# Kernel tuning notes

Measured on AMD Instinct MI355X. Metric: run time of the kernel, lower is better.

The kernel has to match this reference:

```python
import jax, jax.numpy as jnp
import numpy as np

D_MODEL = 1024
N_HEADS = 16
D_K = D_MODEL // N_HEADS
NEG_INF = -1e30


def setup_inputs() -> dict:
    key = jax.random.key(0)
    ks = jax.random.split(key, 12)
    B, S = 4, 2048
    scale = 1.0 / np.sqrt(D_MODEL)
    inp = {
        "query": jax.random.normal(ks[0], (B, S, D_MODEL), jnp.float32),
        "key": jax.random.normal(ks[1], (B, S, D_MODEL), jnp.float32),
        "value": jax.random.normal(ks[2], (B, S, D_MODEL), jnp.float32),
        "mask": jax.random.randint(ks[3], (B, S, S), 0, 2, jnp.int32),
        "w_q": jax.random.normal(ks[4], (D_MODEL, D_MODEL), jnp.float32) * scale,
        "b_q": jnp.zeros((D_MODEL,), jnp.float32),
        "w_k": jax.random.normal(ks[5], (D_MODEL, D_MODEL), jnp.float32) * scale,
        "b_k": jnp.zeros((D_MODEL,), jnp.float32),
        "w_v": jax.random.normal(ks[6], (D_MODEL, D_MODEL), jnp.float32) * scale,
        "b_v": jnp.zeros((D_MODEL,), jnp.float32),
        "w_o": jax.random.normal(ks[7], (D_MODEL, D_MODEL), jnp.float32) * scale,
        "b_o": jnp.zeros((D_MODEL,), jnp.float32),
    }
    return inp


def reference(query, key, value, mask, w_q, b_q, w_k, b_k, w_v, b_v, w_o, b_o):
    B, Sq, _ = query.shape
    Sk = key.shape[1]
    # Linear projections (torch nn.Linear: x @ W.T + b), split into heads
    Q = (query @ w_q.T + b_q).reshape(B, Sq, N_HEADS, D_K).transpose(0, 2, 1, 3)
    K = (key @ w_k.T + b_k).reshape(B, Sk, N_HEADS, D_K).transpose(0, 2, 1, 3)
    V = (value @ w_v.T + b_v).reshape(B, Sk, N_HEADS, D_K).transpose(0, 2, 1, 3)
    # scores: (B, H, Sq, Sk)
    scores = jnp.einsum('bhqd,bhkd->bhqk', Q, K) / jnp.sqrt(jnp.float32(D_K))
    scores = jnp.where(mask[:, None, :, :] == 0, NEG_INF, scores)
    attn = jax.nn.softmax(scores, axis=-1)  # dropout p=0 -> identity (eval)
    context = jnp.einsum('bhqk,bhkd->bhqd', attn, V)
    context = context.transpose(0, 2, 1, 3).reshape(B, Sq, D_MODEL)
    return context @ w_o.T + b_o
```

## Files before the change

### kernel.cpp

```cpp
#include <hip/hip_runtime.h>
#include <hip/hip_bf16.h>
#include <stdint.h>

#define DM 1024
#define NHEADS 16
#define DK 64
#define BB 4
#define SS 2048

typedef unsigned short u16;
typedef __bf16 bf16x8 __attribute__((ext_vector_type(8)));
typedef __bf16 bf16x4 __attribute__((ext_vector_type(4)));
typedef float f32x4 __attribute__((ext_vector_type(4)));

#if __has_builtin(__builtin_amdgcn_exp2f)
#define EXP2(x) __builtin_amdgcn_exp2f(x)
#else
#define EXP2(x) exp2f(x)
#endif

static __device__ __forceinline__ u16 f2bf(float f) {
    union { float f; uint32_t u; } v; v.f = f;
    uint32_t r = v.u + 0x7fffu + ((v.u >> 16) & 1u);
    return (u16)(r >> 16);
}

static __device__ __forceinline__ f32x4 mfma16(bf16x8 a, bf16x8 b, f32x4 c) {
    return __builtin_amdgcn_mfma_f32_16x16x32_bf16(a, b, c, 0, 0, 0);
}

static __device__ __forceinline__ void gload16(const u16* g, u16* l) {
    __builtin_amdgcn_global_load_lds((const __attribute__((address_space(1))) void*)g,
                                     (__attribute__((address_space(3))) void*)l, 16, 0, 0);
}

#define PREP_W 4096
#define PREP_X 12288
#define PREP_M 2048
__global__ __launch_bounds__(256) void k_prep(const float* __restrict__ wq, const float* __restrict__ wk,
                                              const float* __restrict__ wv, const float* __restrict__ wo,
                                              u16* __restrict__ wout,
                                              const float* __restrict__ xq, const float* __restrict__ xk,
                                              const float* __restrict__ xv, u16* __restrict__ xout,
                                              const int* __restrict__ mask, uint32_t* __restrict__ bits) {
    const int bid = blockIdx.x, tid = threadIdx.x;
    if (bid < PREP_W) {
        int t = bid * 256 + tid;
        int which = t >> 18;
        int off = (t & 0x3FFFF) << 2;
        const float* src = (which == 0) ? wq : (which == 1) ? wk : (which == 2) ? wv : wo;
        float4 v = *(const float4*)(src + off);
        ushort4 o;
        o.x = f2bf(v.x); o.y = f2bf(v.y); o.z = f2bf(v.z); o.w = f2bf(v.w);
        *(ushort4*)(wout + ((size_t)which << 20) + off) = o;
    } else if (bid < PREP_W + PREP_X) {
        int lb = bid - PREP_W;
        int which = lb >> 12;
        const float* src = (which == 0) ? xq : (which == 1) ? xk : xv;
        size_t base = (((size_t)(lb & 4095)) * 256 + tid) * 8;
        float4 v0 = *(const float4*)(src + base);
        float4 v1 = *(const float4*)(src + base + 4);
        union { u16 s[8]; uint4 u; } p;
        p.s[0]=f2bf(v0.x); p.s[1]=f2bf(v0.y); p.s[2]=f2bf(v0.z); p.s[3]=f2bf(v0.w);
        p.s[4]=f2bf(v1.x); p.s[5]=f2bf(v1.y); p.s[6]=f2bf(v1.z); p.s[7]=f2bf(v1.w);
        *(uint4*)(xout + ((size_t)which << 23) + base) = p.u;
    } else {
        int lb = bid - PREP_W - PREP_X;
        int gid = lb * 256 + tid;
        int lane = gid & 63;
        int wv_ = gid >> 6;
        const int nw = (PREP_M * 256) >> 6;
        const long totalInts = (long)BB * SS * SS;
        for (long base = (long)wv_ * 64; base < totalInts; base += (long)nw * 64) {
            int m = mask[base + lane];
            unsigned long long bal = __ballot(m != 0);
            if (lane == 0)  bits[(base >> 5)]     = (uint32_t)bal;
            if (lane == 32) bits[(base >> 5) + 1] = (uint32_t)(bal >> 32);
        }
    }
}

template<int MODE>
static __device__ __forceinline__ void gemm256(const u16* __restrict__ X, const u16* __restrict__ W,
                                               const float* __restrict__ bias, void* __restrict__ Yv,
                                               float alpha, int tile, int tid,
                                               u16* __restrict__ Ab, u16* __restrict__ Bb) {
    const int lane = tid & 63, w = tid >> 6;
    const int wr = w >> 1, wc = w & 1;
    const int lrow = lane & 15, lgrp = lane >> 4;
    const int m0 = (tile >> 3) * 256;
    const int n0 = (tile & 7) * 128;
    const int srow = tid >> 2;
    const int scol = (tid & 3) * 8;

    f32x4 acc[4][4] = {};

    for (int kk = 0; kk < DM; kk += 32) {
        gload16(X + (size_t)(m0 + srow) * DM + kk + scol,       &Ab[tid * 8]);
        gload16(X + (size_t)(m0 + 128 + srow) * DM + kk + scol, &Ab[4096 + tid * 8]);
        gload16(W + (size_t)(n0 + srow) * DM + kk + scol,       &Bb[tid * 8]);
        __syncthreads();
        bf16x8 af[4], bfr[4];
#pragma unroll
        for (int i = 0; i < 4; ++i)
            af[i] = *(const bf16x8*)&Ab[(wr * 64 + i * 16 + lrow) * 32 + lgrp * 8];
#pragma unroll
        for (int j = 0; j < 4; ++j)
            bfr[j] = *(const bf16x8*)&Bb[(wc * 64 + j * 16 + lrow) * 32 + lgrp * 8];
#pragma unroll
        for (int i = 0; i < 4; ++i)
#pragma unroll
            for (int j = 0; j < 4; ++j)
                acc[i][j] = mfma16(af[i], bfr[j], acc[i][j]);
        __syncthreads();
    }

#pragma unroll
    for (int j = 0; j < 4; ++j) {
        int n = n0 + wc * 64 + j * 16 + lrow;
        float bv_ = bias[n];
        int h = n >> 6, d = n & 63;
#pragma unroll
        for (int i = 0; i < 4; ++i) {
            int mbase = m0 + wr * 64 + i * 16 + (lgrp << 2);
            if (MODE == 0) {
                u16* Y = (u16*)Yv;
#pragma unroll
                for (int r = 0; r < 4; ++r) {
                    int m = mbase + r;
                    int b = m >> 11, s = m & 2047;
                    Y[(((size_t)(b * NHEADS + h) * SS) + s) * DK + d] = f2bf((acc[i][j][r] + bv_) * alpha);
                }
            } else if (MODE == 1) {
                int b = mbase >> 11, s = mbase & 2047;
                ushort4 o;
                o.x = f2bf(acc[i][j][0] + bv_);
                o.y = f2bf(acc[i][j][1] + bv_);
                o.z = f2bf(acc[i][j][2] + bv_);
                o.w = f2bf(acc[i][j][3] + bv_);
                *(ushort4*)&((u16*)Yv)[(((size_t)(b * NHEADS + h) * DK) + d) * SS + s] = o;
            } else {
                float* Y = (float*)Yv;
#pragma unroll
                for (int r = 0; r < 4; ++r)
                    Y[(size_t)(mbase + r) * DM + n] = acc[i][j][r] + bv_;
            }
        }
    }
}

__global__ __launch_bounds__(512, 4) void k_projqkv(const u16* __restrict__ Xq, const u16* __restrict__ Xk,
                                                    const u16* __restrict__ Xv, const u16* __restrict__ Wb,
                                                    const float* __restrict__ bq, const float* __restrict__ bk,
                                                    const float* __restrict__ bv,
                                                    u16* __restrict__ Qw, u16* __restrict__ Kw,
                                                    u16* __restrict__ Vw, float qscale) {
    __shared__ u16 Ab[256 * 32];
    __shared__ u16 Bb[128 * 32];
    const int sel = blockIdx.x >> 8;
    const int tile = blockIdx.x & 255;
    if (sel == 0)      gemm256<0>(Xq, Wb,               bq, Qw, qscale, tile, threadIdx.x, Ab, Bb);
    else if (sel == 1) gemm256<0>(Xk, Wb + (1u << 20),  bk, Kw, 1.0f,   tile, threadIdx.x, Ab, Bb);
    else               gemm256<1>(Xv, Wb + (2u << 20),  bv, Vw, 1.0f,   tile, threadIdx.x, Ab, Bb);
}

__global__ __launch_bounds__(512, 4) void k_oproj(const u16* __restrict__ X, const u16* __restrict__ W,
                                                  const float* __restrict__ bias, float* __restrict__ out) {
    __shared__ u16 Ab[256 * 32];
    __shared__ u16 Bb[128 * 32];
    gemm256<2>(X, W, bias, out, 1.0f, blockIdx.x, threadIdx.x, Ab, Bb);
}

#define NT (SS / 64)
__global__ __launch_bounds__(512, 4) void k_attn(const u16* __restrict__ Q, const u16* __restrict__ K,
                                                 const u16* __restrict__ VT, const uint32_t* __restrict__ mbits,
                                                 u16* __restrict__ ctx) {
    __shared__ u16 Kt[2][64 * 64];
    __shared__ u16 Vt[2][64 * 64];
    __shared__ u16 Pl[8][16][72];
    const int tid = threadIdx.x;
    const int lane = tid & 63, w = tid >> 6;
    const int lrow = lane & 15, lgrp = lane >> 4;
    const int bid = blockIdx.x;
    const int bh = bid & 63;
    const int qt = bid >> 6;
    const int b = bh >> 4, h = bh & 15;
    const int qbase = qt * 128 + w * 16;

    const u16* Qh = Q + (size_t)bh * SS * DK;
    const u16* Kh = K + (size_t)bh * SS * DK;
    const u16* Vh = VT + (size_t)bh * DK * SS;

    bf16x8 qf0, qf1;
    {
        const u16* p = Qh + (size_t)(qbase + lrow) * DK + lgrp * 8;
        qf0 = *(const bf16x8*)(p);
        qf1 = *(const bf16x8*)(p + 32);
    }

    const uint64_t* mrow = (const uint64_t*)mbits + ((size_t)(b * SS + qbase + lrow)) * (SS / 64);

    union { uint4 u; bf16x8 v; } onesu;
    onesu.u = make_uint4(0x3F803F80u, 0x3F803F80u, 0x3F803F80u, 0x3F803F80u);
    const bf16x8 ones = onesu.v;

    const int swzA = (lgrp * 8) ^ ((lrow & 7) * 8);
    const int swzB = (32 + lgrp * 8) ^ ((lrow & 7) * 8);

    const int srow = tid >> 3;
    const int ssrc = ((tid & 7) * 8) ^ ((srow & 7) * 8);

    f32x4 acc[4] = {};
    f32x4 asum = {};

    gload16(Kh + (size_t)srow * DK + ssrc, &Kt[0][tid * 8]);
    gload16(Vh + (size_t)srow * SS + ssrc, &Vt[0][tid * 8]);
    __syncthreads();

    int cur = 0;
    for (int kt = 0; kt < NT; ++kt) {
        if (kt + 1 < NT) {
            gload16(Kh + (size_t)((kt + 1) * 64 + srow) * DK + ssrc, &Kt[cur ^ 1][tid * 8]);
            gload16(Vh + (size_t)srow * SS + (kt + 1) * 64 + ssrc, &Vt[cur ^ 1][tid * 8]);
        }
        const uint64_t wm = mrow[kt];

        const u16* Kc = Kt[cur];
        const u16* Vc = Vt[cur];
        f32x4 st[4] = {};
#pragma unroll
        for (int t = 0; t < 4; ++t) {
            bf16x8 ka = *(const bf16x8*)&Kc[(16 * t + lrow) * 64 + swzA];
            bf16x8 kb = *(const bf16x8*)&Kc[(16 * t + lrow) * 64 + swzB];
            st[t] = mfma16(ka, qf0, st[t]);
            st[t] = mfma16(kb, qf1, st[t]);
        }
#pragma unroll
        for (int t = 0; t < 4; ++t) {
            uint32_t wt = (uint32_t)(wm >> (16 * t + 4 * lgrp));
            bf16x4 pk;
#pragma unroll
            for (int r = 0; r < 4; ++r) {
                float p = EXP2(st[t][r]);
                p = ((wt >> r) & 1u) ? p : 0.0f;
                pk[r] = (__bf16)p;
            }
            *(bf16x4*)&Pl[w][lrow][16 * t + 4 * lgrp] = pk;
        }
        bf16x8 pf0 = *(const bf16x8*)&Pl[w][lrow][lgrp * 8];
        bf16x8 pf1 = *(const bf16x8*)&Pl[w][lrow][32 + lgrp * 8];
        asum = mfma16(pf0, ones, asum);
        asum = mfma16(pf1, ones, asum);
#pragma unroll
        for (int dt = 0; dt < 4; ++dt) {
            bf16x8 vf0 = *(const bf16x8*)&Vc[(16 * dt + lrow) * 64 + swzA];
            bf16x8 vf1 = *(const bf16x8*)&Vc[(16 * dt + lrow) * 64 + swzB];
            acc[dt] = mfma16(pf0, vf0, acc[dt]);
            acc[dt] = mfma16(pf1, vf1, acc[dt]);
        }
        __syncthreads();
        cur ^= 1;
    }

#pragma unroll
    for (int r = 0; r < 4; ++r) {
        float li = 1.0f / asum[r];
        int q = qbase + 4 * lgrp + r;
#pragma unroll
        for (int dt = 0; dt < 4; ++dt)
            ctx[((size_t)b * SS + q) * DM + h * 64 + dt * 16 + lrow] = f2bf(acc[dt][r] * li);
    }
}

extern "C" void kernel_launch(void* const* d_in, const int* in_sizes, int n_in,
                              void* d_out, int out_size, void* d_ws, size_t ws_size,
                              hipStream_t stream) {
    const float* query = (const float*)d_in[0];
    const float* key   = (const float*)d_in[1];
    const float* value = (const float*)d_in[2];
    const int*   mask  = (const int*)d_in[3];
    const float* w_q   = (const float*)d_in[4];
    const float* b_q   = (const float*)d_in[5];
    const float* w_k   = (const float*)d_in[6];
    const float* b_k   = (const float*)d_in[7];
    const float* w_v   = (const float*)d_in[8];
    const float* b_v   = (const float*)d_in[9];
    const float* w_o   = (const float*)d_in[10];
    const float* b_o   = (const float*)d_in[11];
    float* out = (float*)d_out;

    char* ws = (char*)d_ws;
    u16*      Wb = (u16*)(ws);
    uint32_t* mb = (uint32_t*)(ws + (8u  << 20));
    u16*      Xq = (u16*)(ws + (16u << 20));
    u16*      Xk = (u16*)(ws + (32u << 20));
    u16*      Xv = (u16*)(ws + (48u << 20));
    u16*      Qw = (u16*)(ws + (64u << 20));
    u16*      Kw = (u16*)(ws + (80u << 20));
    u16*      Vw = (u16*)(ws + (96u << 20));
    u16*      Cw = (u16*)(ws + (112u << 20));

    const float qscale = 0.125f * 1.4426950408889634f;

    k_prep<<<dim3(PREP_W + PREP_X + PREP_M), dim3(256), 0, stream>>>(
        w_q, w_k, w_v, w_o, Wb, query, key, value, Xq, mask, mb);
    k_projqkv<<<dim3(768), dim3(512), 0, stream>>>(Xq, Xk, Xv, Wb, b_q, b_k, b_v,
                                                   Qw, Kw, Vw, qscale);
    k_attn<<<dim3(1024), dim3(512), 0, stream>>>(Qw, Kw, Vw, mb, Cw);
    k_oproj<<<dim3(256), dim3(512), 0, stream>>>(Cw, Wb + (3u << 20), b_o, out);
}
```

Before: 289.5 us.

## Retile projection GEMMs to 128x128 with K=64 steps and swizzled LDS

```diff
diff --git a/kernel.cpp b/kernel.cpp
--- a/kernel.cpp
+++ b/kernel.cpp
@@ -81,37 +81,44 @@
 }
 
 template<int MODE>
-static __device__ __forceinline__ void gemm256(const u16* __restrict__ X, const u16* __restrict__ W,
+static __device__ __forceinline__ void gemm128(const u16* __restrict__ X, const u16* __restrict__ W,
                                                const float* __restrict__ bias, void* __restrict__ Yv,
                                                float alpha, int tile, int tid,
                                                u16* __restrict__ Ab, u16* __restrict__ Bb) {
     const int lane = tid & 63, w = tid >> 6;
     const int wr = w >> 1, wc = w & 1;
     const int lrow = lane & 15, lgrp = lane >> 4;
-    const int m0 = (tile >> 3) * 256;
+    const int m0 = (tile >> 3) * 128;
     const int n0 = (tile & 7) * 128;
-    const int srow = tid >> 2;
-    const int scol = (tid & 3) * 8;
+    const int sr = tid >> 3;
+    const int scol = (((tid & 7) ^ (sr & 7)) * 8);
+    const int rswz = (lrow & 7) * 8;
 
     f32x4 acc[4][4] = {};
 
-    for (int kk = 0; kk < DM; kk += 32) {
-        gload16(X + (size_t)(m0 + srow) * DM + kk + scol,       &Ab[tid * 8]);
-        gload16(X + (size_t)(m0 + 128 + srow) * DM + kk + scol, &Ab[4096 + tid * 8]);
-        gload16(W + (size_t)(n0 + srow) * DM + kk + scol,       &Bb[tid * 8]);
+    for (int kk = 0; kk < DM; kk += 64) {
+#pragma unroll
+        for (int i = 0; i < 4; ++i) {
+            int row = i * 32 + sr;
+            gload16(X + (size_t)(m0 + row) * DM + kk + scol, &Ab[i * 2048 + tid * 8]);
+            gload16(W + (size_t)(n0 + row) * DM + kk + scol, &Bb[i * 2048 + tid * 8]);
+        }
         __syncthreads();
-        bf16x8 af[4], bfr[4];
-#pragma unroll
-        for (int i = 0; i < 4; ++i)
-            af[i] = *(const bf16x8*)&Ab[(wr * 64 + i * 16 + lrow) * 32 + lgrp * 8];
-#pragma unroll
-        for (int j = 0; j < 4; ++j)
-            bfr[j] = *(const bf16x8*)&Bb[(wc * 64 + j * 16 + lrow) * 32 + lgrp * 8];
-#pragma unroll
-        for (int i = 0; i < 4; ++i)
+#pragma unroll
+        for (int kh = 0; kh < 2; ++kh) {
+            bf16x8 af[4], bfr[4];
+#pragma unroll
+            for (int i = 0; i < 4; ++i)
+                af[i] = *(const bf16x8*)&Ab[(wr * 64 + i * 16 + lrow) * 64 + ((kh * 32 + lgrp * 8) ^ rswz)];
 #pragma unroll
             for (int j = 0; j < 4; ++j)
-                acc[i][j] = mfma16(af[i], bfr[j], acc[i][j]);
+                bfr[j] = *(const bf16x8*)&Bb[(wc * 64 + j * 16 + lrow) * 64 + ((kh * 32 + lgrp * 8) ^ rswz)];
+#pragma unroll
+            for (int i = 0; i < 4; ++i)
+#pragma unroll
+                for (int j = 0; j < 4; ++j)
+                    acc[i][j] = mfma16(af[i], bfr[j], acc[i][j]);
+        }
         __syncthreads();
     }
 
@@ -149,26 +156,26 @@
     }
 }
 
-__global__ __launch_bounds__(512, 4) void k_projqkv(const u16* __restrict__ Xq, const u16* __restrict__ Xk,
-                                                    const u16* __restrict__ Xv, const u16* __restrict__ Wb,
-                                                    const float* __restrict__ bq, const float* __restrict__ bk,
-                                                    const float* __restrict__ bv,
-                                                    u16* __restrict__ Qw, u16* __restrict__ Kw,
-                                                    u16* __restrict__ Vw, float qscale) {
-    __shared__ u16 Ab[256 * 32];
-    __shared__ u16 Bb[128 * 32];
-    const int sel = blockIdx.x >> 8;
-    const int tile = blockIdx.x & 255;
-    if (sel == 0)      gemm256<0>(Xq, Wb,               bq, Qw, qscale, tile, threadIdx.x, Ab, Bb);
-    else if (sel == 1) gemm256<0>(Xk, Wb + (1u << 20),  bk, Kw, 1.0f,   tile, threadIdx.x, Ab, Bb);
-    else               gemm256<1>(Xv, Wb + (2u << 20),  bv, Vw, 1.0f,   tile, threadIdx.x, Ab, Bb);
-}
-
-__global__ __launch_bounds__(512, 4) void k_oproj(const u16* __restrict__ X, const u16* __restrict__ W,
-                                                  const float* __restrict__ bias, float* __restrict__ out) {
-    __shared__ u16 Ab[256 * 32];
-    __shared__ u16 Bb[128 * 32];
-    gemm256<2>(X, W, bias, out, 1.0f, blockIdx.x, threadIdx.x, Ab, Bb);
+__global__ __launch_bounds__(256) void k_projqkv(const u16* __restrict__ Xq, const u16* __restrict__ Xk,
+                                                 const u16* __restrict__ Xv, const u16* __restrict__ Wb,
+                                                 const float* __restrict__ bq, const float* __restrict__ bk,
+                                                 const float* __restrict__ bv,
+                                                 u16* __restrict__ Qw, u16* __restrict__ Kw,
+                                                 u16* __restrict__ Vw, float qscale) {
+    __shared__ u16 Ab[128 * 64];
+    __shared__ u16 Bb[128 * 64];
+    const int sel = blockIdx.x >> 9;
+    const int tile = blockIdx.x & 511;
+    if (sel == 0)      gemm128<0>(Xq, Wb,              bq, Qw, qscale, tile, threadIdx.x, Ab, Bb);
+    else if (sel == 1) gemm128<0>(Xk, Wb + (1u << 20), bk, Kw, 1.0f,   tile, threadIdx.x, Ab, Bb);
+    else               gemm128<1>(Xv, Wb + (2u << 20), bv, Vw, 1.0f,   tile, threadIdx.x, Ab, Bb);
+}
+
+__global__ __launch_bounds__(256) void k_oproj(const u16* __restrict__ X, const u16* __restrict__ W,
+                                               const float* __restrict__ bias, float* __restrict__ out) {
+    __shared__ u16 Ab[128 * 64];
+    __shared__ u16 Bb[128 * 64];
+    gemm128<2>(X, W, bias, out, 1.0f, blockIdx.x, threadIdx.x, Ab, Bb);
 }
 
 #define NT (SS / 64)
@@ -304,8 +311,8 @@
 
     k_prep<<<dim3(PREP_W + PREP_X + PREP_M), dim3(256), 0, stream>>>(
         w_q, w_k, w_v, w_o, Wb, query, key, value, Xq, mask, mb);
-    k_projqkv<<<dim3(768), dim3(512), 0, stream>>>(Xq, Xk, Xv, Wb, b_q, b_k, b_v,
-                                                   Qw, Kw, Vw, qscale);
+    k_projqkv<<<dim3(1536), dim3(256), 0, stream>>>(Xq, Xk, Xv, Wb, b_q, b_k, b_v,
+                                                    Qw, Kw, Vw, qscale);
     k_attn<<<dim3(1024), dim3(512), 0, stream>>>(Qw, Kw, Vw, mb, Cw);
-    k_oproj<<<dim3(256), dim3(512), 0, stream>>>(Cw, Wb + (3u << 20), b_o, out);
-}
+    k_oproj<<<dim3(512), dim3(256), 0, stream>>>(Cw, Wb + (3u << 20), b_o, out);
+}
```

After: 265.0 us. -8.5%, faster.
